# Kernel optimization log

Measured on AMD Instinct MI355X. Metric: run time of the kernel, lower is better.

## Reference

```python
import jax, jax.numpy as jnp
import numpy as np

SHUFFLE_G = 8
NUM_HEADS = 8
EPS = 1e-12


def setup_inputs() -> dict:
    key = jax.random.key(0)
    ks = jax.random.split(key, 7)
    b, dim, t, h, w = 2, 64, 10, 128, 128
    c3 = dim * 3
    return {
        "x": jax.random.normal(ks[0], (b, dim, t, h, w), jnp.float32),
        "W1": jax.random.normal(ks[1], (c3, dim), jnp.float32) * 0.05,            # 1x1x1 conv
        "Wdw": jax.random.normal(ks[2], (c3, 1, 1, 3, 3), jnp.float32) * 0.1,     # depthwise (1,3,3) conv
        "W_lin": jax.random.normal(ks[3], (t * SHUFFLE_G, t * SHUFFLE_G), jnp.float32) * 0.05,
        "b_lin": jax.random.normal(ks[4], (t * SHUFFLE_G,), jnp.float32) * 0.01,
        "temperature": jnp.ones((NUM_HEADS, 1, 1), jnp.float32),
        "W_out": jax.random.normal(ks[5], (dim, dim), jnp.float32) * 0.05,        # 1x1x1 conv
    }


def _l2norm(v):
    n = jnp.sqrt(jnp.sum(v * v, axis=-1, keepdims=True))
    return v / jnp.maximum(n, EPS)


def reference(x, W1, Wdw, W_lin, b_lin, temperature, W_out):
    b, c, t, h, w = x.shape
    c3 = 3 * c
    heads = NUM_HEADS
    # 1x1x1 pointwise conv (no bias)
    y = jnp.einsum('oc,bcthw->bothw', W1, x)
    # depthwise (1,3,3) conv, padding (0,1,1)
    y = jax.lax.conv_general_dilated(
        y, Wdw, window_strides=(1, 1, 1),
        padding=((0, 0), (1, 1), (1, 1)),
        dimension_numbers=('NCDHW', 'OIDHW', 'NCDHW'),
        feature_group_count=c3)
    # shuffle: b (c1 c2) t h w -> b c2 h w (c1 t), c1 = SHUFFLE_G
    c1, c2 = SHUFFLE_G, c3 // SHUFFLE_G
    y = y.reshape(b, c1, c2, t, h, w).transpose(0, 2, 4, 5, 1, 3).reshape(b, c2, h, w, c1 * t)
    # linear mixing along (c1 t)
    y = jnp.einsum('bchwi,oi->bchwo', y, W_lin) + b_lin
    # unshuffle: b c2 h w (c1 t) -> b (c2 c1 t) h w
    y = y.reshape(b, c2, h, w, c1, t).transpose(0, 1, 4, 5, 2, 3).reshape(b, c3 * t, h, w)
    # split qkv along channel
    q, k, v = jnp.split(y, 3, axis=1)  # each [b, c*t, h, w]
    ct, hw = (c // heads) * t, h * w
    q = q.reshape(b, heads, ct, hw)
    k = k.reshape(b, heads, ct, hw)
    v = v.reshape(b, heads, ct, hw)
    q = _l2norm(q)
    k = _l2norm(k)
    attn = jnp.einsum('bhcd,bhed->bhce', q, k) * temperature  # [b, heads, ct, ct]
    attn = jax.nn.softmax(attn, axis=-1)
    out = jnp.einsum('bhce,bhed->bhcd', attn, v)  # [b, heads, ct, hw]
    out = out.reshape(b, c, t, h, w)
    out = jnp.einsum('oc,bcthw->bothw', W_out, out)
    return out
```

## Files before the change

### kernel.cpp

```cpp
#include <hip/hip_runtime.h>
#include <hip/hip_bf16.h>

#define C_  64
#define C3_ 192
#define T_  10
#define H_  128
#define W_  128
#define HW_ 16384
#define THW_ 163840
#define NH_ 8
#define C2_ 24
#define TG_ 80

typedef __hip_bfloat16 bf16;
typedef __attribute__((ext_vector_type(8))) short bf16x8;
typedef __attribute__((ext_vector_type(4))) float f32x4;

__device__ __forceinline__ float bf2f(bf16 v) { return __bfloat162float(v); }

__device__ __forceinline__ ushort f2bf_s(float f) {
  bf16 h = __float2bfloat16(f);
  union { bf16 b; ushort s; } u; u.b = h; return u.s;
}

__device__ __forceinline__ ushort4 pack4(f32x4 a) {
  ushort4 p;
  p.x = f2bf_s(a[0]); p.y = f2bf_s(a[1]); p.z = f2bf_s(a[2]); p.w = f2bf_s(a[3]);
  return p;
}

__device__ __forceinline__ uint pack2lo(uint x, uint y) { return (x & 0xffffu) | (y << 16); }
__device__ __forceinline__ uint pack2hi(uint x, uint y) { return (x >> 16) | (y & 0xffff0000u); }

__device__ __forceinline__ void twrite(char* lds, int stride, int nkc,
                                       uint r[8][4], int kc, int cg) {
#pragma unroll
  for (int j = 0; j < 8; ++j) {
    const int d = j >> 1;
    uint4 o;
    if (j & 1) {
      o.x = pack2hi(r[0][d], r[1][d]); o.y = pack2hi(r[2][d], r[3][d]);
      o.z = pack2hi(r[4][d], r[5][d]); o.w = pack2hi(r[6][d], r[7][d]);
    } else {
      o.x = pack2lo(r[0][d], r[1][d]); o.y = pack2lo(r[2][d], r[3][d]);
      o.z = pack2lo(r[4][d], r[5][d]); o.w = pack2lo(r[6][d], r[7][d]);
    }
    const int col = cg * 8 + j;
    const int rr = (kc + col) % nkc;
    *reinterpret_cast<uint4*>(lds + col * stride + rr * 16) = o;
  }
}

__global__ __launch_bounds__(256) void kprep(
    const float* __restrict__ W1, const float* __restrict__ W_lin,
    const float* __restrict__ W_out,
    bf16* __restrict__ W1bf, bf16* __restrict__ Wlinbf, bf16* __restrict__ Woutbf) {
  const int idx = blockIdx.x * 256 + threadIdx.x;
  if (idx < 12288) {
    W1bf[idx] = __float2bfloat16(W1[idx]);
  } else if (idx < 12288 + 7680) {
    const int i = idx - 12288;
    const int row = i / 96, col = i - row * 96;
    Wlinbf[i] = __float2bfloat16(col < 80 ? W_lin[row * 80 + col] : 0.f);
  } else if (idx < 12288 + 7680 + 4096) {
    const int i = idx - 12288 - 7680;
    Woutbf[i] = __float2bfloat16(W_out[i]);
  }
}

__global__ __launch_bounds__(256, 5) void k1_mfma(
    const float* __restrict__ x, const bf16* __restrict__ W1bf,
    bf16* __restrict__ y1ws) {
  __shared__ __align__(16) float xs[64 * 128];
  const int tid = threadIdx.x;
  const int lane = tid & 63, wv = tid >> 6;
  const int lr = lane & 15, lg = lane >> 4;
  const int mh = blockIdx.y;
  const int b = blockIdx.z;
  const float* xb = x + (size_t)b * C_ * THW_;
  bf16* y1 = y1ws + (size_t)b * C3_ * THW_;
  const int n0 = blockIdx.x * 128;

  {
    const int ro = lane >> 5, colo = (lane & 31) * 4;
#pragma unroll
    for (int i = 0; i < 8; ++i) {
      const int row = wv * 16 + i * 2;
      const int rr = row + ro;
      const int sw = (rr >> 3) & 1;
      const float* gsrc = xb + (size_t)rr * THW_ + n0 + (colo ^ (sw << 4));
      __builtin_amdgcn_global_load_lds(
          (const __attribute__((address_space(1))) void*)gsrc,
          (__attribute__((address_space(3))) void*)&xs[row * 128],
          16, 0, 0);
    }
  }

  bf16x8 wf[6][2];
#pragma unroll
  for (int mt = 0; mt < 6; ++mt)
#pragma unroll
    for (int c = 0; c < 2; ++c) {
      const int row = mh * 96 + mt * 16 + lr;
      wf[mt][c] = *reinterpret_cast<const bf16x8*>(W1bf + row * 64 + c * 32 + lg * 8);
    }
  __syncthreads();

#pragma unroll
  for (int nt = 0; nt < 2; ++nt) {
    const int col = wv * 32 + nt * 16 + lr;
    const int col2 = col ^ ((lg & 1) << 4);
    bf16x8 xa[2];
#pragma unroll
    for (int c = 0; c < 2; ++c) {
      const float* base = &xs[(c * 32 + lg * 8) * 128 + col2];
      bf16x8 f;
#pragma unroll
      for (int e = 0; e < 8; ++e) f[e] = f2bf_s(base[e * 128]);
      xa[c] = f;
    }
    f32x4 acc[6];
#pragma unroll
    for (int mt = 0; mt < 6; ++mt) acc[mt] = (f32x4){0.f, 0.f, 0.f, 0.f};
#pragma unroll
    for (int c = 0; c < 2; ++c)
#pragma unroll
      for (int mt = 0; mt < 6; ++mt)
        acc[mt] = __builtin_amdgcn_mfma_f32_16x16x32_bf16(xa[c], wf[mt][c], acc[mt], 0, 0, 0);
    const int nb = n0 + wv * 32 + nt * 16 + lg * 4;
#pragma unroll
    for (int mt = 0; mt < 6; ++mt) {
      const int o = mh * 96 + mt * 16 + lr;
      *reinterpret_cast<ushort4*>(y1 + (size_t)o * THW_ + nb) = pack4(acc[mt]);
    }
  }
}

__global__ __launch_bounds__(256) void k2_dw(
    const bf16* __restrict__ y1ws, const float* __restrict__ Wdw,
    bf16* __restrict__ y2ws) {
  __shared__ float tile[34][132];
  const int tid = threadIdx.x;
  const int blk = blockIdx.x;
  const int b = blockIdx.y;
  const bf16* y1 = y1ws + (size_t)b * C3_ * THW_;
  bf16* y2 = y2ws + (size_t)b * C3_ * THW_;
  const int hs = (blk & 3) * 32;
  const int rest = blk >> 2;
  const int t = rest % T_;
  const int o = rest / T_;
  const bf16* src = y1 + ((size_t)o * T_ + t) * HW_;

  if (tid < 68) {
    const int r = tid >> 1, side = tid & 1;
    tile[r][side ? 129 : 0] = 0.f;
  }
  {
    const int rr = tid >> 5, c4 = (tid & 31) * 4;
#pragma unroll
    for (int p = 0; p < 5; ++p) {
      const int r = p * 8 + rr;
      if (r < 34) {
        const int hh = hs - 1 + r;
        float e0 = 0.f, e1 = 0.f, e2 = 0.f, e3 = 0.f;
        if (hh >= 0 && hh < H_) {
          uint2 raw = *reinterpret_cast<const uint2*>(src + hh * W_ + c4);
          e0 = __uint_as_float(raw.x << 16);
          e1 = __uint_as_float(raw.x & 0xffff0000u);
          e2 = __uint_as_float(raw.y << 16);
          e3 = __uint_as_float(raw.y & 0xffff0000u);
        }
        tile[r][1 + c4]     = e0;
        tile[r][1 + c4 + 1] = e1;
        tile[r][1 + c4 + 2] = e2;
        tile[r][1 + c4 + 3] = e3;
      }
    }
  }
  __syncthreads();

  float kk[9];
#pragma unroll
  for (int i = 0; i < 9; ++i) kk[i] = Wdw[o * 9 + i];

  bf16* dst = y2 + ((size_t)o * T_ + t) * HW_;
  const int w = tid & 127;
  const int r0 = (tid >> 7) * 16;

  float a[3][3];
#pragma unroll
  for (int ky = 0; ky < 3; ++ky)
#pragma unroll
    for (int kx = 0; kx < 3; ++kx) a[ky][kx] = tile[r0 + ky][w + kx];

#pragma unroll
  for (int q = 0; q < 16; ++q) {
    float acc = 0.f;
#pragma unroll
    for (int ky = 0; ky < 3; ++ky)
#pragma unroll
      for (int kx = 0; kx < 3; ++kx)
        acc = fmaf(kk[ky * 3 + kx], a[ky][kx], acc);
    dst[(hs + r0 + q) * W_ + w] = __float2bfloat16(acc);
    if (q < 15) {
#pragma unroll
      for (int kx = 0; kx < 3; ++kx) {
        a[0][kx] = a[1][kx];
        a[1][kx] = a[2][kx];
        a[2][kx] = tile[r0 + q + 3][w + kx];
      }
    }
  }
}

#define K3_NKC 13
#define K3_STRIDE 208
#define K3_TPB 4
#define CB_S 136
__global__ __launch_bounds__(256) void k3_mfma(
    const bf16* __restrict__ y2ws, const bf16* __restrict__ Wlinbf,
    const float* __restrict__ b_lin, bf16* __restrict__ zws,
    float* __restrict__ ssqws) {
  __shared__ __align__(16) char lds[256 * K3_STRIDE];
  __shared__ __align__(16) ushort cbuf[80 * CB_S];
  const int tid = threadIdx.x;
  const int tile0 = blockIdx.x * K3_TPB;
  const int c2 = blockIdx.y;
  const int b = blockIdx.z;
  const bf16* y2 = y2ws + (size_t)b * C3_ * THW_;
  bf16* z = zws + (size_t)b * C3_ * THW_;
  float* ssq = ssqws + b * 1280;

  const int lane = tid & 63, wv = tid >> 6;
  const int lr = lane & 15, lg = lane >> 4;

  const int kcA = tid >> 5, cgA = tid & 31;
  const bool hasB = (tid & 3) == 0;
  const int qB = tid >> 2;
  const int kcB = 8 + (qB >> 5), cgB = qB & 31;

  uint rrA[8][4], rrB[8][4];
  auto LOAD = [&](int s0, uint r[8][4], int kc, int cg) {
#pragma unroll
    for (int e = 0; e < 8; ++e) {
      const int k = kc * 8 + e;
      const int c1 = (k * 205) >> 11;
      const int tt = k - c1 * 10;
      uint4 raw = *reinterpret_cast<const uint4*>(
          y2 + ((size_t)((c1 * C2_ + c2) * T_ + tt)) * HW_ + s0 + cg * 8);
      r[e][0] = raw.x; r[e][1] = raw.y; r[e][2] = raw.z; r[e][3] = raw.w;
    }
  };

  LOAD(tile0 * 256, rrA, kcA, cgA);
  if (hasB) LOAD(tile0 * 256, rrB, kcB, cgB);
  {
    const int col = tid;
    const uint4 zero4 = {0, 0, 0, 0};
    *reinterpret_cast<uint4*>(lds + col * K3_STRIDE + ((10 + col) % K3_NKC) * 16) = zero4;
    *reinterpret_cast<uint4*>(lds + col * K3_STRIDE + ((11 + col) % K3_NKC) * 16) = zero4;
  }

  bf16x8 wf[5][3];
#pragma unroll
  for (int mt = 0; mt < 5; ++mt)
#pragma unroll
    for (int c = 0; c < 3; ++c)
      wf[mt][c] = *reinterpret_cast<const bf16x8*>(
          Wlinbf + (mt * 16 + lr) * 96 + c * 32 + lg * 8);
  float bias[5];
#pragma unroll
  for (int mt = 0; mt < 5; ++mt) bias[mt] = b_lin[mt * 16 + lr];

  float sqp[5] = {0.f, 0.f, 0.f, 0.f, 0.f};

#pragma unroll
  for (int t = 0; t < K3_TPB; ++t) {
    const int s0 = (tile0 + t) * 256;
    twrite(lds, K3_STRIDE, K3_NKC, rrA, kcA, cgA);
    if (hasB) twrite(lds, K3_STRIDE, K3_NKC, rrB, kcB, cgB);
    __syncthreads();
    if (t + 1 < K3_TPB) {
      LOAD(s0 + 256, rrA, kcA, cgA);
      if (hasB) LOAD(s0 + 256, rrB, kcB, cgB);
    }

#pragma unroll
    for (int p = 0; p < 2; ++p) {
      f32x4 acc2[2][5];
#pragma unroll
      for (int nth = 0; nth < 2; ++nth) {
        const int nt = p * 2 + nth;
        const int col = wv * 64 + nt * 16 + lr;
        bf16x8 xa[3];
#pragma unroll
        for (int c = 0; c < 3; ++c) {
          const int kc = c * 4 + lg;
          xa[c] = *reinterpret_cast<const bf16x8*>(
              lds + col * K3_STRIDE + ((kc + col) % K3_NKC) * 16);
        }
#pragma unroll
        for (int mt = 0; mt < 5; ++mt)
          acc2[nth][mt] = (f32x4){bias[mt], bias[mt], bias[mt], bias[mt]};
#pragma unroll
        for (int c = 0; c < 3; ++c)
#pragma unroll
          for (int mt = 0; mt < 5; ++mt)
            acc2[nth][mt] = __builtin_amdgcn_mfma_f32_16x16x32_bf16(
                xa[c], wf[mt][c], acc2[nth][mt], 0, 0, 0);
#pragma unroll
        for (int mt = 0; mt < 5; ++mt)
#pragma unroll
          for (int j = 0; j < 4; ++j)
            sqp[mt] = fmaf(acc2[nth][mt][j], acc2[nth][mt][j], sqp[mt]);
      }
#pragma unroll
      for (int nth = 0; nth < 2; ++nth)
#pragma unroll
        for (int mt = 0; mt < 5; ++mt)
          *reinterpret_cast<ushort4*>(
              &cbuf[(mt * 16 + lr) * CB_S + wv * 32 + nth * 16 + lg * 4]) =
              pack4(acc2[nth][mt]);
      __syncthreads();
#pragma unroll
      for (int i = 0; i < 5; ++i) {
        const int q = i * 256 + tid;
        const int row = q >> 4, cch = q & 15;
        uint4 v = *reinterpret_cast<const uint4*>(&cbuf[row * CB_S + cch * 8]);
        const int u = c2 * TG_ + row;
        const int gcol = s0 + (cch >> 2) * 64 + p * 32 + (cch & 3) * 8;
        *reinterpret_cast<uint4*>(z + (size_t)u * HW_ + gcol) = v;
      }
      __syncthreads();
    }
  }

  if (c2 < 16) {
#pragma unroll
    for (int mt = 0; mt < 5; ++mt) {
      float v = sqp[mt];
      v += __shfl_xor(v, 16);
      v += __shfl_xor(v, 32);
      if (lane < 16)
        atomicAdd(&ssq[c2 * TG_ + mt * 16 + lane], v);
    }
  }
}

__global__ __launch_bounds__(256) void k5_mfma(
    const bf16* __restrict__ zws, float* __restrict__ Gpartws) {
  __shared__ __align__(16) float gbuf[2][TG_ * TG_];
  const int chunk = blockIdx.x, h = blockIdx.y, b = blockIdx.z;
  const bf16* z = zws + (size_t)b * C3_ * THW_;
  float* Gpart = Gpartws + (size_t)b * 819200;
  const int tid = threadIdx.x;
  const int lane = tid & 63, wv = tid >> 6;
  const int lr = lane & 15, lg = lane >> 4;

  const bf16* qbase = z + (size_t)(h * TG_) * HW_;
  const bf16* kbase = z + (size_t)((8 + h) * TG_) * HW_;

  f32x4 acc[5][5];
#pragma unroll
  for (int a = 0; a < 5; ++a)
#pragma unroll
    for (int b2 = 0; b2 < 5; ++b2) acc[a][b2] = (f32x4){0.f, 0.f, 0.f, 0.f};

  const int s0 = chunk * 1024 + wv * 256;
  for (int s = s0; s < s0 + 256; s += 32) {
    bf16x8 qa[5], kb[5];
#pragma unroll
    for (int a = 0; a < 5; ++a)
      qa[a] = *reinterpret_cast<const bf16x8*>(qbase + (size_t)(a * 16 + lr) * HW_ + s + lg * 8);
#pragma unroll
    for (int a = 0; a < 5; ++a)
      kb[a] = *reinterpret_cast<const bf16x8*>(kbase + (size_t)(a * 16 + lr) * HW_ + s + lg * 8);
#pragma unroll
    for (int a = 0; a < 5; ++a)
#pragma unroll
      for (int b2 = 0; b2 < 5; ++b2)
        acc[a][b2] = __builtin_amdgcn_mfma_f32_16x16x32_bf16(qa[a], kb[b2], acc[a][b2], 0, 0, 0);
  }

  if (wv == 1 || wv == 3) {
    float* dst = gbuf[wv >> 1];
#pragma unroll
    for (int a = 0; a < 5; ++a)
#pragma unroll
      for (int b2 = 0; b2 < 5; ++b2)
#pragma unroll
        for (int j = 0; j < 4; ++j)
          dst[(a * 16 + lg * 4 + j) * TG_ + b2 * 16 + lr] = acc[a][b2][j];
  }
  __syncthreads();
  if (wv == 0 || wv == 2) {
    const float* srcb = gbuf[wv >> 1];
#pragma unroll
    for (int a = 0; a < 5; ++a)
#pragma unroll
      for (int b2 = 0; b2 < 5; ++b2)
#pragma unroll
        for (int j = 0; j < 4; ++j)
          acc[a][b2][j] += srcb[(a * 16 + lg * 4 + j) * TG_ + b2 * 16 + lr];
  }
  __syncthreads();
  if (wv == 2) {
#pragma unroll
    for (int a = 0; a < 5; ++a)
#pragma unroll
      for (int b2 = 0; b2 < 5; ++b2)
#pragma unroll
        for (int j = 0; j < 4; ++j)
          gbuf[0][(a * 16 + lg * 4 + j) * TG_ + b2 * 16 + lr] = acc[a][b2][j];
  }
  __syncthreads();
  if (wv == 0) {
    float* gp = Gpart + ((size_t)chunk * 8 + h) * TG_ * TG_;
#pragma unroll
    for (int a = 0; a < 5; ++a)
#pragma unroll
      for (int b2 = 0; b2 < 5; ++b2)
#pragma unroll
        for (int j = 0; j < 4; ++j) {
          const int i = a * 16 + lg * 4 + j, jj = b2 * 16 + lr;
          gp[i * TG_ + jj] = acc[a][b2][j] + gbuf[0][i * TG_ + jj];
        }
  }
}

__global__ __launch_bounds__(128) void k6_softmax(
    const float* __restrict__ Gpartws, const float* __restrict__ ssqws,
    const float* __restrict__ temp, bf16* __restrict__ attnbfws) {
  __shared__ float red[128];
  __shared__ float smax, ssum;
  const int b = blockIdx.y;
  const float* Gpart = Gpartws + (size_t)b * 819200;
  const float* ssq = ssqws + b * 1280;
  bf16* attnbf = attnbfws + (size_t)b * NH_ * TG_ * 96;
  int h = blockIdx.x / TG_, i = blockIdx.x % TG_;
  int j = threadIdx.x;
  float logit = -1e30f;
  if (j < TG_) {
    float g = 0.f;
    for (int c = 0; c < 16; ++c)
      g += Gpart[(((size_t)c * 8 + h) * TG_ + i) * TG_ + j];
    float nq = ssq[h * TG_ + i];
    float nk = ssq[(8 + h) * TG_ + j];
    float sq = 1.f / fmaxf(sqrtf(nq), 1e-12f);
    float sk = 1.f / fmaxf(sqrtf(nk), 1e-12f);
    logit = g * sq * sk * temp[h];
  }
  red[j] = logit;
  __syncthreads();
  if (j == 0) {
    float m = -1e30f;
    for (int x2 = 0; x2 < TG_; ++x2) m = fmaxf(m, red[x2]);
    smax = m;
  }
  __syncthreads();
  float e = (j < TG_) ? expf(logit - smax) : 0.f;
  red[j] = e;
  __syncthreads();
  if (j == 0) {
    float s = 0.f;
    for (int x2 = 0; x2 < TG_; ++x2) s += red[x2];
    ssum = s;
  }
  __syncthreads();
  if (j < 96)
    attnbf[((size_t)h * TG_ + i) * 96 + j] =
        __float2bfloat16(j < TG_ ? e / ssum : 0.f);
}

#define K7A_TPB 2
__global__ __launch_bounds__(256) void k7a_mfma(
    const bf16* __restrict__ zws, const bf16* __restrict__ attnbfws,
    bf16* __restrict__ att_outws) {
  __shared__ __align__(16) char lds[256 * K3_STRIDE];
  __shared__ __align__(16) ushort cbuf[80 * CB_S];
  const int tid = threadIdx.x;
  const int tile0 = blockIdx.x * K7A_TPB;
  const int h = blockIdx.y;
  const int b = blockIdx.z;
  const bf16* z = zws + (size_t)b * C3_ * THW_;
  const bf16* attnbf = attnbfws + (size_t)b * NH_ * TG_ * 96;
  bf16* att_out = att_outws + (size_t)b * NH_ * TG_ * HW_;
  const int voff = (16 + h) * TG_;

  const int lane = tid & 63, wv = tid >> 6;
  const int lr = lane & 15, lg = lane >> 4;

  const int kcA = tid >> 5, cgA = tid & 31;
  const bool hasB = (tid & 3) == 0;
  const int qB = tid >> 2;
  const int kcB = 8 + (qB >> 5), cgB = qB & 31;

  uint rrA[8][4], rrB[8][4];
  auto LOAD = [&](int s0, uint r[8][4], int kc, int cg) {
#pragma unroll
    for (int e = 0; e < 8; ++e) {
      uint4 raw = *reinterpret_cast<const uint4*>(
          z + (size_t)(voff + kc * 8 + e) * HW_ + s0 + cg * 8);
      r[e][0] = raw.x; r[e][1] = raw.y; r[e][2] = raw.z; r[e][3] = raw.w;
    }
  };

  LOAD(tile0 * 256, rrA, kcA, cgA);
  if (hasB) LOAD(tile0 * 256, rrB, kcB, cgB);
  {
    const int col = tid;
    const uint4 zero4 = {0, 0, 0, 0};
    *reinterpret_cast<uint4*>(lds + col * K3_STRIDE + ((10 + col) % K3_NKC) * 16) = zero4;
    *reinterpret_cast<uint4*>(lds + col * K3_STRIDE + ((11 + col) % K3_NKC) * 16) = zero4;
  }

  bf16x8 wf[5][3];
#pragma unroll
  for (int mt = 0; mt < 5; ++mt)
#pragma unroll
    for (int c = 0; c < 3; ++c)
      wf[mt][c] = *reinterpret_cast<const bf16x8*>(
          attnbf + ((size_t)h * TG_ + mt * 16 + lr) * 96 + c * 32 + lg * 8);

#pragma unroll
  for (int t = 0; t < K7A_TPB; ++t) {
    const int s0 = (tile0 + t) * 256;
    twrite(lds, K3_STRIDE, K3_NKC, rrA, kcA, cgA);
    if (hasB) twrite(lds, K3_STRIDE, K3_NKC, rrB, kcB, cgB);
    __syncthreads();
    if (t + 1 < K7A_TPB) {
      LOAD(s0 + 256, rrA, kcA, cgA);
      if (hasB) LOAD(s0 + 256, rrB, kcB, cgB);
    }

#pragma unroll
    for (int p = 0; p < 2; ++p) {
      f32x4 acc2[2][5];
#pragma unroll
      for (int nth = 0; nth < 2; ++nth) {
        const int nt = p * 2 + nth;
        const int col = wv * 64 + nt * 16 + lr;
        bf16x8 xa[3];
#pragma unroll
        for (int c = 0; c < 3; ++c) {
          const int kc = c * 4 + lg;
          xa[c] = *reinterpret_cast<const bf16x8*>(
              lds + col * K3_STRIDE + ((kc + col) % K3_NKC) * 16);
        }
#pragma unroll
        for (int mt = 0; mt < 5; ++mt) acc2[nth][mt] = (f32x4){0.f, 0.f, 0.f, 0.f};
#pragma unroll
        for (int c = 0; c < 3; ++c)
#pragma unroll
          for (int mt = 0; mt < 5; ++mt)
            acc2[nth][mt] = __builtin_amdgcn_mfma_f32_16x16x32_bf16(
                xa[c], wf[mt][c], acc2[nth][mt], 0, 0, 0);
      }
#pragma unroll
      for (int nth = 0; nth < 2; ++nth)
#pragma unroll
        for (int mt = 0; mt < 5; ++mt)
          *reinterpret_cast<ushort4*>(
              &cbuf[(mt * 16 + lr) * CB_S + wv * 32 + nth * 16 + lg * 4]) =
              pack4(acc2[nth][mt]);
      __syncthreads();
#pragma unroll
      for (int i = 0; i < 5; ++i) {
        const int q = i * 256 + tid;
        const int row = q >> 4, cch = q & 15;
        uint4 v = *reinterpret_cast<const uint4*>(&cbuf[row * CB_S + cch * 8]);
        const int u = h * TG_ + row;
        const int gcol = s0 + (cch >> 2) * 64 + p * 32 + (cch & 3) * 8;
        *reinterpret_cast<uint4*>(att_out + (size_t)u * HW_ + gcol) = v;
      }
      __syncthreads();
    }
  }
}

#define K1_NKC 10
#define K1_STRIDE 160
#define K7B_TPB 2
__global__ __launch_bounds__(256) void k7b_mfma(
    const bf16* __restrict__ att_outws, const bf16* __restrict__ Woutbf,
    float* __restrict__ out) {
  __shared__ __align__(16) char lds[256 * K1_STRIDE];
  const int tid = threadIdx.x;
  const int tile0 = blockIdx.x * K7B_TPB;
  const int b = blockIdx.y;
  const bf16* att_out = att_outws + (size_t)b * NH_ * TG_ * HW_;
  float* outb = out + (size_t)b * C_ * THW_;
  const int t_ = tile0 >> 6;
  const int lane = tid & 63, wv = tid >> 6;
  const int lr = lane & 15, lg = lane >> 4;

  const int kcA = tid >> 5, cgA = tid & 31;
  uint rrA[8][4];
  auto LOAD = [&](int tile, uint r[8][4]) {
    const int sb0 = (tile * 256) & (HW_ - 1);
#pragma unroll
    for (int e = 0; e < 8; ++e) {
      const int row = kcA * TG_ + e * T_ + t_;
      uint4 raw = *reinterpret_cast<const uint4*>(
          att_out + (size_t)row * HW_ + sb0 + cgA * 8);
      r[e][0] = raw.x; r[e][1] = raw.y; r[e][2] = raw.z; r[e][3] = raw.w;
    }
  };

  LOAD(tile0, rrA);

  bf16x8 wf[4][2];
#pragma unroll
  for (int mt = 0; mt < 4; ++mt)
#pragma unroll
    for (int c = 0; c < 2; ++c)
      wf[mt][c] = *reinterpret_cast<const bf16x8*>(
          Woutbf + (mt * 16 + lr) * 64 + c * 32 + lg * 8);

#pragma unroll
  for (int t = 0; t < K7B_TPB; ++t) {
    const int n0 = (tile0 + t) * 256;
    twrite(lds, K1_STRIDE, K1_NKC, rrA, kcA, cgA);
    __syncthreads();
    if (t + 1 < K7B_TPB) LOAD(tile0 + t + 1, rrA);

    for (int nt = 0; nt < 4; ++nt) {
      const int col = wv * 64 + nt * 16 + lr;
      bf16x8 xa[2];
#pragma unroll
      for (int c = 0; c < 2; ++c) {
        const int kc = c * 4 + lg;
        xa[c] = *reinterpret_cast<const bf16x8*>(
            lds + col * K1_STRIDE + ((kc + col) % K1_NKC) * 16);
      }
      f32x4 acc[4];
#pragma unroll
      for (int mt = 0; mt < 4; ++mt) acc[mt] = (f32x4){0.f, 0.f, 0.f, 0.f};
#pragma unroll
      for (int c = 0; c < 2; ++c)
#pragma unroll
        for (int mt = 0; mt < 4; ++mt)
          acc[mt] = __builtin_amdgcn_mfma_f32_16x16x32_bf16(xa[c], wf[mt][c], acc[mt], 0, 0, 0);
      const int nb = n0 + wv * 64 + nt * 16 + lg * 4;
#pragma unroll
      for (int mt = 0; mt < 4; ++mt) {
        const int o = mt * 16 + lr;
        *reinterpret_cast<float4*>(outb + (size_t)o * THW_ + nb) =
            (float4){acc[mt][0], acc[mt][1], acc[mt][2], acc[mt][3]};
      }
    }
    __syncthreads();
  }
}

extern "C" void kernel_launch(void* const* d_in, const int* in_sizes, int n_in,
                              void* d_out, int out_size, void* d_ws, size_t ws_size,
                              hipStream_t stream) {
  const float* x    = (const float*)d_in[0];
  const float* W1   = (const float*)d_in[1];
  const float* Wdw  = (const float*)d_in[2];
  const float* Wlin = (const float*)d_in[3];
  const float* blin = (const float*)d_in[4];
  const float* temp = (const float*)d_in[5];
  const float* Wout = (const float*)d_in[6];
  float* out = (float*)d_out;

  const size_t NY = (size_t)C3_ * THW_;
  char* ws = (char*)d_ws;
  bf16* y1z = (bf16*)ws;
  bf16* y2  = (bf16*)(ws + 4 * NY);
  char* E   = ws + 8 * NY;
  float* Gpart  = (float*)E;
  bf16* attnbf  = (bf16*)(E + 6553600);
  bf16* att_out = (bf16*)(E + 7045120);
  float* ssq    = (float*)(E + 48988160);
  bf16* W1bf    = (bf16*)(E + 48998400);
  bf16* Wlinbf  = (bf16*)(E + 49022976);
  bf16* Woutbf  = (bf16*)(E + 49038336);

  kprep<<<94, 256, 0, stream>>>(W1, Wlin, Wout, W1bf, Wlinbf, Woutbf);
  hipMemsetAsync(ssq, 0, 2 * 1280 * sizeof(float), stream);
  k1_mfma<<<dim3(THW_ / 128, 2, 2), 256, 0, stream>>>(x, W1bf, y1z);
  k2_dw<<<dim3(C3_ * T_ * 4, 2), 256, 0, stream>>>(y1z, Wdw, y2);
  k3_mfma<<<dim3(HW_ / 256 / K3_TPB, C2_, 2), 256, 0, stream>>>(y2, Wlinbf, blin, y1z, ssq);
  k5_mfma<<<dim3(16, NH_, 2), 256, 0, stream>>>(y1z, Gpart);
  k6_softmax<<<dim3(NH_ * TG_, 2), 128, 0, stream>>>(Gpart, ssq, temp, attnbf);
  k7a_mfma<<<dim3(HW_ / 256 / K7A_TPB, NH_, 2), 256, 0, stream>>>(y1z, attnbf, att_out);
  k7b_mfma<<<dim3(THW_ / 256 / K7B_TPB, 2), 256, 0, stream>>>(att_out, Woutbf, out);
}
```

Measured before the change: 271.2 us.

## Double-buffer x tiles in pointwise conv kernel and fold ssq memset into prep

The 1x1x1 conv kernel now handles four column tiles per block and prefetches the next tile into a second LDS buffer via async global-to-LDS loads while computing the current one. W1 fragments stay in registers across those tiles. The separate memset of the sum-of-squares buffer is folded into the weight prep kernel, removing one launch. LDS use per block doubles to 64KB and the occupancy hint is dropped, so fewer blocks may be resident per CU.

```diff
diff --git a/kernel.cpp b/kernel.cpp
--- a/kernel.cpp
+++ b/kernel.cpp
@@ -54,8 +54,10 @@
 __global__ __launch_bounds__(256) void kprep(
     const float* __restrict__ W1, const float* __restrict__ W_lin,
     const float* __restrict__ W_out,
-    bf16* __restrict__ W1bf, bf16* __restrict__ Wlinbf, bf16* __restrict__ Woutbf) {
+    bf16* __restrict__ W1bf, bf16* __restrict__ Wlinbf, bf16* __restrict__ Woutbf,
+    float* __restrict__ ssq) {
   const int idx = blockIdx.x * 256 + threadIdx.x;
+  if (idx < 2560) ssq[idx] = 0.f;
   if (idx < 12288) {
     W1bf[idx] = __float2bfloat16(W1[idx]);
   } else if (idx < 12288 + 7680) {
@@ -68,10 +70,11 @@
   }
 }
 
-__global__ __launch_bounds__(256, 5) void k1_mfma(
+#define K1_TPB 4
+__global__ __launch_bounds__(256) void k1_mfma(
     const float* __restrict__ x, const bf16* __restrict__ W1bf,
     bf16* __restrict__ y1ws) {
-  __shared__ __align__(16) float xs[64 * 128];
+  __shared__ __align__(16) float xs[2][64 * 128];
   const int tid = threadIdx.x;
   const int lane = tid & 63, wv = tid >> 6;
   const int lr = lane & 15, lg = lane >> 4;
@@ -79,10 +82,11 @@
   const int b = blockIdx.z;
   const float* xb = x + (size_t)b * C_ * THW_;
   bf16* y1 = y1ws + (size_t)b * C3_ * THW_;
-  const int n0 = blockIdx.x * 128;
-
-  {
-    const int ro = lane >> 5, colo = (lane & 31) * 4;
+  const int tile0 = blockIdx.x * K1_TPB;
+
+  const int ro = lane >> 5, colo = (lane & 31) * 4;
+  auto STAGE = [&](int buf, int tIdx) {
+    const int n0 = tIdx * 128;
 #pragma unroll
     for (int i = 0; i < 8; ++i) {
       const int row = wv * 16 + i * 2;
@@ -91,10 +95,12 @@
       const float* gsrc = xb + (size_t)rr * THW_ + n0 + (colo ^ (sw << 4));
       __builtin_amdgcn_global_load_lds(
           (const __attribute__((address_space(1))) void*)gsrc,
-          (__attribute__((address_space(3))) void*)&xs[row * 128],
+          (__attribute__((address_space(3))) void*)&xs[buf][row * 128],
           16, 0, 0);
     }
-  }
+  };
+
+  STAGE(0, tile0);
 
   bf16x8 wf[6][2];
 #pragma unroll
@@ -106,33 +112,40 @@
     }
   __syncthreads();
 
-#pragma unroll
-  for (int nt = 0; nt < 2; ++nt) {
-    const int col = wv * 32 + nt * 16 + lr;
-    const int col2 = col ^ ((lg & 1) << 4);
-    bf16x8 xa[2];
-#pragma unroll
-    for (int c = 0; c < 2; ++c) {
-      const float* base = &xs[(c * 32 + lg * 8) * 128 + col2];
-      bf16x8 f;
-#pragma unroll
-      for (int e = 0; e < 8; ++e) f[e] = f2bf_s(base[e * 128]);
-      xa[c] = f;
-    }
-    f32x4 acc[6];
-#pragma unroll
-    for (int mt = 0; mt < 6; ++mt) acc[mt] = (f32x4){0.f, 0.f, 0.f, 0.f};
-#pragma unroll
-    for (int c = 0; c < 2; ++c)
-#pragma unroll
-      for (int mt = 0; mt < 6; ++mt)
-        acc[mt] = __builtin_amdgcn_mfma_f32_16x16x32_bf16(xa[c], wf[mt][c], acc[mt], 0, 0, 0);
-    const int nb = n0 + wv * 32 + nt * 16 + lg * 4;
-#pragma unroll
-    for (int mt = 0; mt < 6; ++mt) {
-      const int o = mh * 96 + mt * 16 + lr;
-      *reinterpret_cast<ushort4*>(y1 + (size_t)o * THW_ + nb) = pack4(acc[mt]);
-    }
+  int buf = 0;
+  for (int t = 0; t < K1_TPB; ++t) {
+    if (t + 1 < K1_TPB) STAGE(buf ^ 1, tile0 + t + 1);
+    const int n0 = (tile0 + t) * 128;
+#pragma unroll
+    for (int nt = 0; nt < 2; ++nt) {
+      const int col = wv * 32 + nt * 16 + lr;
+      const int col2 = col ^ ((lg & 1) << 4);
+      bf16x8 xa[2];
+#pragma unroll
+      for (int c = 0; c < 2; ++c) {
+        const float* base = &xs[buf][(c * 32 + lg * 8) * 128 + col2];
+        bf16x8 f;
+#pragma unroll
+        for (int e = 0; e < 8; ++e) f[e] = f2bf_s(base[e * 128]);
+        xa[c] = f;
+      }
+      f32x4 acc[6];
+#pragma unroll
+      for (int mt = 0; mt < 6; ++mt) acc[mt] = (f32x4){0.f, 0.f, 0.f, 0.f};
+#pragma unroll
+      for (int c = 0; c < 2; ++c)
+#pragma unroll
+        for (int mt = 0; mt < 6; ++mt)
+          acc[mt] = __builtin_amdgcn_mfma_f32_16x16x32_bf16(xa[c], wf[mt][c], acc[mt], 0, 0, 0);
+      const int nb = n0 + wv * 32 + nt * 16 + lg * 4;
+#pragma unroll
+      for (int mt = 0; mt < 6; ++mt) {
+        const int o = mh * 96 + mt * 16 + lr;
+        *reinterpret_cast<ushort4*>(y1 + (size_t)o * THW_ + nb) = pack4(acc[mt]);
+      }
+    }
+    __syncthreads();
+    buf ^= 1;
   }
 }
 
@@ -678,9 +691,8 @@
   bf16* Wlinbf  = (bf16*)(E + 49022976);
   bf16* Woutbf  = (bf16*)(E + 49038336);
 
-  kprep<<<94, 256, 0, stream>>>(W1, Wlin, Wout, W1bf, Wlinbf, Woutbf);
-  hipMemsetAsync(ssq, 0, 2 * 1280 * sizeof(float), stream);
-  k1_mfma<<<dim3(THW_ / 128, 2, 2), 256, 0, stream>>>(x, W1bf, y1z);
+  kprep<<<94, 256, 0, stream>>>(W1, Wlin, Wout, W1bf, Wlinbf, Woutbf, ssq);
+  k1_mfma<<<dim3(THW_ / 128 / K1_TPB, 2, 2), 256, 0, stream>>>(x, W1bf, y1z);
   k2_dw<<<dim3(C3_ * T_ * 4, 2), 256, 0, stream>>>(y1z, Wdw, y2);
   k3_mfma<<<dim3(HW_ / 256 / K3_TPB, C2_, 2), 256, 0, stream>>>(y2, Wlinbf, blin, y1z, ssq);
   k5_mfma<<<dim3(16, NH_, 2), 256, 0, stream>>>(y1z, Gpart);
```

Result: faster. 256.6 us (-5.4%).
